# Performance work log

Measured on AMD Instinct MI355X. Metric: run time of the kernel, lower is better.

Reference implementation:

```python
import jax, jax.numpy as jnp
import numpy as np

T, LDIMS, HID, HID2 = 768, 256, 512, 512


def setup_inputs() -> dict:
    key = jax.random.key(0)
    ks = jax.random.split(key, 8)
    s = 0.05  # small init scale keeps tanh out of saturation
    return {
        "x": jax.random.normal(ks[0], (T, 2, LDIMS), dtype=jnp.float32),
        "hidLayerFOH": jax.random.normal(ks[1], (2 * LDIMS, HID), dtype=jnp.float32) * s,
        "hidLayerFOM": jax.random.normal(ks[2], (2 * LDIMS, HID), dtype=jnp.float32) * s,
        "catBias": jax.random.normal(ks[3], (2 * HID,), dtype=jnp.float32) * s,
        "hid2Layer": jax.random.normal(ks[4], (2 * HID, HID2), dtype=jnp.float32) * s,
        "hid2Bias": jax.random.normal(ks[5], (HID2,), dtype=jnp.float32) * s,
        "outLayer": jax.random.normal(ks[6], (HID2, 1), dtype=jnp.float32) * s,
        "outBias": jax.random.normal(ks[7], (1,), dtype=jnp.float32) * s,
    }


def reference(x, hidLayerFOH, hidLayerFOM, catBias, hid2Layer, hid2Bias, outLayer, outBias):
    # x: [T, 2, ldims] -> concat forward/backward LSTM states -> [T, 2*ldims]
    xc = x.reshape(x.shape[0], -1)
    Hf = xc @ hidLayerFOH  # [T, HID] headfov per token
    Mf = xc @ hidLayerFOM  # [T, HID] modfov per token
    # Original: tanh(concat([headfov_i, modfov_j]) + catBias) @ hid2Layer.
    # tanh is elementwise, so split the concat: act halves separately, then
    # split hid2Layer into top/bottom blocks — same math, no [T,T,2H] tensor.
    actH = jnp.tanh(Hf + catBias[:HID])   # [T, HID]
    actM = jnp.tanh(Mf + catBias[HID:])   # [T, HID]
    AH = actH @ hid2Layer[:HID]           # [T, HID2]
    AM = actM @ hid2Layer[HID:]           # [T, HID2]
    # Pairwise second layer: Z[i,j] = tanh(AH[i] + AM[j] + hid2Bias)
    Z = jnp.tanh(AH[:, None, :] + AM[None, :, :] + hid2Bias)  # [T, T, HID2]
    scores = jnp.einsum("ijh,h->ij", Z, outLayer[:, 0]) + outBias[0]  # [T, T]
    return scores
```

## Files before the change

kernel.cpp:

```cpp
#include <hip/hip_runtime.h>

#define TT 768
#define KD 512
#define NC 1024
#define RLN2_2 2.8853900817779268f

typedef short short8 __attribute__((ext_vector_type(8)));
typedef float f32x4  __attribute__((ext_vector_type(4)));
typedef float f32x2  __attribute__((ext_vector_type(2)));

__device__ __forceinline__ float fast_exp2(float x) {
#if __has_builtin(__builtin_amdgcn_exp2f)
    return __builtin_amdgcn_exp2f(x);
#else
    return exp2f(x);
#endif
}
__device__ __forceinline__ float fast_rcp(float x) {
#if __has_builtin(__builtin_amdgcn_rcpf)
    return __builtin_amdgcn_rcpf(x);
#else
    return 1.0f / x;
#endif
}
__device__ __forceinline__ float fast_tanh(float x) {
    float e = fast_exp2(x * RLN2_2);
    return fmaf(-2.0f, fast_rcp(e + 1.0f), 1.0f);
}
__device__ __forceinline__ ushort f2bf(float f) {
    uint u = __float_as_uint(f);
    u += 0x7fff + ((u >> 16) & 1);
    return (ushort)(u >> 16);
}

__global__ __launch_bounds__(128) void k_gemm1(
    const float* __restrict__ x, const float* __restrict__ foh,
    const float* __restrict__ fom, const float* __restrict__ catBias,
    ushort* __restrict__ act)
{
    __shared__ float ps[64][20];
    __shared__ float bt[2][32][33];

    const int t = threadIdx.x;
    const int kv = t >> 6, lane = t & 63;
    const int n0 = blockIdx.x * 32;
    const int m0 = blockIdx.y * 32;
    const float* B = (n0 < 512) ? foh : fom;
    const int nc0  = (n0 < 512) ? n0 : n0 - 512;
    const int lrow = lane & 15, lk = (lane >> 4) * 8;
    const int kbase = kv * 256;

    const int skr = lane >> 1;
    const int snc = (lane & 1) * 16;

    const float* px0 = &x[(m0 + lrow) * KD + kbase + lk];
    const float* px1 = px0 + 16 * KD;

    f32x4 acc[2][2] = {};
    #pragma unroll 1
    for (int c = 0; c < 8; ++c) {
        const int k0 = kbase + c * 32;
        const float* bsrc = &B[(k0 + skr) * 512 + nc0 + snc];
        float4 s0 = *(const float4*)(bsrc);
        float4 s1 = *(const float4*)(bsrc + 4);
        float4 s2 = *(const float4*)(bsrc + 8);
        float4 s3 = *(const float4*)(bsrc + 12);
        *(float4*)&bt[kv][skr][snc]      = s0;
        *(float4*)&bt[kv][skr][snc + 4]  = s1;
        *(float4*)&bt[kv][skr][snc + 8]  = s2;
        *(float4*)&bt[kv][skr][snc + 12] = s3;
        float4 a00 = *(const float4*)(px0 + c * 32);
        float4 a01 = *(const float4*)(px0 + c * 32 + 4);
        float4 a10 = *(const float4*)(px1 + c * 32);
        float4 a11 = *(const float4*)(px1 + c * 32 + 4);
        short8 af0, af1;
        af0[0] = (short)f2bf(a00.x); af0[1] = (short)f2bf(a00.y);
        af0[2] = (short)f2bf(a00.z); af0[3] = (short)f2bf(a00.w);
        af0[4] = (short)f2bf(a01.x); af0[5] = (short)f2bf(a01.y);
        af0[6] = (short)f2bf(a01.z); af0[7] = (short)f2bf(a01.w);
        af1[0] = (short)f2bf(a10.x); af1[1] = (short)f2bf(a10.y);
        af1[2] = (short)f2bf(a10.z); af1[3] = (short)f2bf(a10.w);
        af1[4] = (short)f2bf(a11.x); af1[5] = (short)f2bf(a11.y);
        af1[6] = (short)f2bf(a11.z); af1[7] = (short)f2bf(a11.w);
        short8 bf0, bf1;
        #pragma unroll
        for (int q = 0; q < 8; ++q) {
            bf0[q] = (short)f2bf(bt[kv][lk + q][lrow]);
            bf1[q] = (short)f2bf(bt[kv][lk + q][lrow + 16]);
        }
        acc[0][0] = __builtin_amdgcn_mfma_f32_16x16x32_bf16(af0, bf0, acc[0][0], 0, 0, 0);
        acc[0][1] = __builtin_amdgcn_mfma_f32_16x16x32_bf16(af0, bf1, acc[0][1], 0, 0, 0);
        acc[1][0] = __builtin_amdgcn_mfma_f32_16x16x32_bf16(af1, bf0, acc[1][0], 0, 0, 0);
        acc[1][1] = __builtin_amdgcn_mfma_f32_16x16x32_bf16(af1, bf1, acc[1][1], 0, 0, 0);
    }
    if (kv == 1) {
        *(f32x4*)&ps[lane][0]  = acc[0][0];
        *(f32x4*)&ps[lane][4]  = acc[0][1];
        *(f32x4*)&ps[lane][8]  = acc[1][0];
        *(f32x4*)&ps[lane][12] = acc[1][1];
    }
    __syncthreads();
    if (kv == 0) {
        acc[0][0] += *(const f32x4*)&ps[lane][0];
        acc[0][1] += *(const f32x4*)&ps[lane][4];
        acc[1][0] += *(const f32x4*)&ps[lane][8];
        acc[1][1] += *(const f32x4*)&ps[lane][12];
        const int crow = (lane >> 4) * 4, ccol = lane & 15;
        #pragma unroll
        for (int nf = 0; nf < 2; ++nf) {
            int col = n0 + nf * 16 + ccol;
            float cb = catBias[col];
            #pragma unroll
            for (int mf = 0; mf < 2; ++mf) {
                #pragma unroll
                for (int r = 0; r < 4; ++r) {
                    int row = m0 + mf * 16 + crow + r;
                    act[row * NC + col] = f2bf(fast_tanh(acc[mf][nf][r] + cb));
                }
            }
        }
    }
}

__global__ __launch_bounds__(128) void k_gemm2(
    const ushort* __restrict__ act, const float* __restrict__ hid2,
    const float* __restrict__ hid2Bias, float* __restrict__ pw)
{
    __shared__ float ps[64][20];
    __shared__ float bt[2][32][33];

    const int t = threadIdx.x;
    const int kv = t >> 6, lane = t & 63;
    const int n0 = blockIdx.x * 32;
    const int m0 = blockIdx.y * 32;
    const bool top = (blockIdx.x < 16);
    const int koff = top ? 0 : 512;
    const int nc0  = top ? n0 : n0 - 512;
    const int lrow = lane & 15, lk = (lane >> 4) * 8;
    const int kbase = kv * 256;

    const int skr = lane >> 1;
    const int snc = (lane & 1) * 16;

    const ushort* pa0 = &act[(m0 + lrow) * NC + koff + kbase + lk];
    const ushort* pa1 = pa0 + 16 * NC;

    f32x4 acc[2][2] = {};
    #pragma unroll 1
    for (int c = 0; c < 8; ++c) {
        const int k0 = kbase + c * 32;
        const float* bsrc = &hid2[(koff + k0 + skr) * 512 + nc0 + snc];
        float4 s0 = *(const float4*)(bsrc);
        float4 s1 = *(const float4*)(bsrc + 4);
        float4 s2 = *(const float4*)(bsrc + 8);
        float4 s3 = *(const float4*)(bsrc + 12);
        *(float4*)&bt[kv][skr][snc]      = s0;
        *(float4*)&bt[kv][skr][snc + 4]  = s1;
        *(float4*)&bt[kv][skr][snc + 8]  = s2;
        *(float4*)&bt[kv][skr][snc + 12] = s3;
        short8 af0 = *(const short8*)(pa0 + c * 32);
        short8 af1 = *(const short8*)(pa1 + c * 32);
        short8 bf0, bf1;
        #pragma unroll
        for (int q = 0; q < 8; ++q) {
            bf0[q] = (short)f2bf(bt[kv][lk + q][lrow]);
            bf1[q] = (short)f2bf(bt[kv][lk + q][lrow + 16]);
        }
        acc[0][0] = __builtin_amdgcn_mfma_f32_16x16x32_bf16(af0, bf0, acc[0][0], 0, 0, 0);
        acc[0][1] = __builtin_amdgcn_mfma_f32_16x16x32_bf16(af0, bf1, acc[0][1], 0, 0, 0);
        acc[1][0] = __builtin_amdgcn_mfma_f32_16x16x32_bf16(af1, bf0, acc[1][0], 0, 0, 0);
        acc[1][1] = __builtin_amdgcn_mfma_f32_16x16x32_bf16(af1, bf1, acc[1][1], 0, 0, 0);
    }
    if (kv == 1) {
        *(f32x4*)&ps[lane][0]  = acc[0][0];
        *(f32x4*)&ps[lane][4]  = acc[0][1];
        *(f32x4*)&ps[lane][8]  = acc[1][0];
        *(f32x4*)&ps[lane][12] = acc[1][1];
    }
    __syncthreads();
    if (kv == 0) {
        acc[0][0] += *(const f32x4*)&ps[lane][0];
        acc[0][1] += *(const f32x4*)&ps[lane][4];
        acc[1][0] += *(const f32x4*)&ps[lane][8];
        acc[1][1] += *(const f32x4*)&ps[lane][12];
        const int crow = (lane >> 4) * 4, ccol = lane & 15;
        #pragma unroll
        for (int nf = 0; nf < 2; ++nf) {
            int col = n0 + nf * 16 + ccol;
            float hb = top ? hid2Bias[col] : 0.0f;
            #pragma unroll
            for (int mf = 0; mf < 2; ++mf) {
                #pragma unroll
                for (int r = 0; r < 4; ++r) {
                    int row = m0 + mf * 16 + crow + r;
                    pw[row * NC + col] = fast_exp2(RLN2_2 * (acc[mf][nf][r] + hb));
                }
            }
        }
    }
}

__global__ __launch_bounds__(256) void k_pair(
    const float* __restrict__ pw, const float* __restrict__ w,
    const float* __restrict__ outBias, float* __restrict__ out)
{
    __shared__ float Ea[4][16][18];
    __shared__ float Em[4][16][18];
    __shared__ float wl[512];

    const int t    = threadIdx.x;
    const int wv   = t >> 6, lane = t & 63;
    const int bid  = blockIdx.x;
    const int sw   = (bid & 7) * 288 + (bid >> 3);
    const int it = sw / 48, jt = sw % 48;
    const int i0 = it * 16, j0 = jt * 16;
    const int hb0 = wv * 128;

    *(float2*)&wl[hb0 + lane * 2] = *(const float2*)&w[hb0 + lane * 2];
    float4 wa = *(const float4*)&w[lane * 8];
    float4 wb = *(const float4*)&w[lane * 8 + 4];
    float lsum = (wa.x + wa.y) + (wa.z + wa.w) + (wb.x + wb.y) + (wb.z + wb.w);
    #pragma unroll
    for (int d = 1; d < 64; d <<= 1) lsum += __shfl_xor(lsum, d, 64);

    const int sr = lane >> 2;
    const int sc = (lane & 3) * 4;
    const float* srcA = &pw[(i0 + sr) * NC + hb0 + sc];
    const float* srcM = &pw[(j0 + sr) * NC + 512 + hb0 + sc];

    const int li = lane >> 3, lj = lane & 7;

    float4 fa = *(const float4*)(srcA);
    float4 fm = *(const float4*)(srcM);

    const f32x2 one2 = {1.0f, 1.0f};
    f32x2 accA[2] = {}, accB[2] = {};

    #pragma unroll 1
    for (int c = 0; c < 8; ++c) {
        const int hh = c * 16;
        *(float4*)&Ea[wv][sr][sc] = fa;
        *(float4*)&Em[wv][sr][sc] = fm;
        if (c < 7) {
            fa = *(const float4*)(srcA + hh + 16);
            fm = *(const float4*)(srcM + hh + 16);
        }
        #pragma unroll
        for (int hq = 0; hq < 4; ++hq) {
            float4 e0 = *(const float4*)&Ea[wv][2 * li    ][hq * 4];
            float4 e1 = *(const float4*)&Ea[wv][2 * li + 1][hq * 4];
            float4 f0 = *(const float4*)&Em[wv][2 * lj    ][hq * 4];
            float4 f1 = *(const float4*)&Em[wv][2 * lj + 1][hq * 4];
            float4 w4 = *(const float4*)&wl[hb0 + hh + hq * 4];
            #define PKQUAD(DA, DB, WH, ACCA, ACCB)                   \
            {                                                        \
                f32x2 Q  = DA * DB;                                  \
                float pr = Q.x * Q.y;                                \
                float R  = fast_rcp(pr);                             \
                float RW = R * (WH);                                 \
                f32x2 T  = (f32x2){Q.y, Q.x} * RW;                   \
                ACCA = __builtin_elementwise_fma(T, DB, ACCA);       \
                ACCB = __builtin_elementwise_fma(T, DA, ACCB);       \
            }
            #define HSTEP(H, S)                                                     \
            {                                                                       \
                f32x2 F  = {f0.H, f1.H};                                            \
                f32x2 D0 = __builtin_elementwise_fma((f32x2){e0.H, e0.H}, F, one2); \
                f32x2 D1 = __builtin_elementwise_fma((f32x2){e1.H, e1.H}, F, one2); \
                PKQUAD(D0, D1, w4.H, accA[S], accB[S])                              \
            }
            HSTEP(x, 0) HSTEP(y, 1) HSTEP(z, 0) HSTEP(w, 1)
            #undef HSTEP
            #undef PKQUAD
        }
    }

    f32x2 s0 = accA[0] + accA[1];
    f32x2 s1 = accB[0] + accB[1];

    float* partial = (float*)Ea;
    __syncthreads();
    if (wv >= 1) {
        float* p = partial + (wv - 1) * 256 + lane * 4;
        p[0] = s0.x; p[1] = s0.y; p[2] = s1.x; p[3] = s1.y;
    }
    __syncthreads();
    if (wv == 0) {
        const float base = lsum + outBias[0];
        float t00 = s0.x, t01 = s0.y, t10 = s1.x, t11 = s1.y;
        #pragma unroll
        for (int q = 0; q < 3; ++q) {
            const float* p = partial + q * 256 + lane * 4;
            t00 += p[0]; t01 += p[1]; t10 += p[2]; t11 += p[3];
        }
        const int gi = i0 + 2 * li, gj = j0 + 2 * lj;
        float2 o0, o1;
        o0.x = fmaf(-2.f, t00, base);
        o0.y = fmaf(-2.f, t01, base);
        o1.x = fmaf(-2.f, t10, base);
        o1.y = fmaf(-2.f, t11, base);
        *(float2*)&out[gi * TT + gj]       = o0;
        *(float2*)&out[(gi + 1) * TT + gj] = o1;
    }
}

extern "C" void kernel_launch(void* const* d_in, const int* in_sizes, int n_in,
                              void* d_out, int out_size, void* d_ws, size_t ws_size,
                              hipStream_t stream) {
    const float* x        = (const float*)d_in[0];
    const float* foh      = (const float*)d_in[1];
    const float* fom      = (const float*)d_in[2];
    const float* catBias  = (const float*)d_in[3];
    const float* hid2     = (const float*)d_in[4];
    const float* hid2Bias = (const float*)d_in[5];
    const float* outLayer = (const float*)d_in[6];
    const float* outBias  = (const float*)d_in[7];
    float* out = (float*)d_out;

    char* wsb = (char*)d_ws;
    float*  pw  = (float*)(wsb);
    ushort* act = (ushort*)(wsb + 3145728);

    k_gemm1<<<dim3(32, 24), 128, 0, stream>>>(x, foh, fom, catBias, act);
    k_gemm2<<<dim3(32, 24), 128, 0, stream>>>(act, hid2, hid2Bias, pw);
    k_pair <<<dim3(2304),   256, 0, stream>>>(pw, outLayer, outBias, out);
}
```

Measured before the change: 55.37 us.

## Enlarge pair tile to 16x32 so each thread computes 2x4 outputs

The pairwise kernel now tiles 16 i-rows by 32 j-columns per block, with each lane computing a 2x4 output patch instead of 2x2, and launches half as many blocks. Each lane reuses the loaded e values across four f values, which cuts shared-memory reads per output and amortizes the weight load and the cross-wave reduction. The rcp-pairing trick now groups the two j-pairs for the same i. The costs are more registers, fewer blocks, and a larger LDS footprint for the Em buffer.

```diff
diff --git a/kernel.cpp b/kernel.cpp
--- a/kernel.cpp
+++ b/kernel.cpp
@@ -205,15 +205,15 @@
     const float* __restrict__ outBias, float* __restrict__ out)
 {
     __shared__ float Ea[4][16][18];
-    __shared__ float Em[4][16][18];
+    __shared__ float Em[4][32][18];
     __shared__ float wl[512];
 
     const int t    = threadIdx.x;
     const int wv   = t >> 6, lane = t & 63;
     const int bid  = blockIdx.x;
-    const int sw   = (bid & 7) * 288 + (bid >> 3);
-    const int it = sw / 48, jt = sw % 48;
-    const int i0 = it * 16, j0 = jt * 16;
+    const int sw   = (bid & 7) * 144 + (bid >> 3);
+    const int it = sw / 24, jt = sw % 24;
+    const int i0 = it * 16, j0 = jt * 32;
     const int hb0 = wv * 128;
 
     *(float2*)&wl[hb0 + lane * 2] = *(const float2*)&w[hb0 + lane * 2];
@@ -223,84 +223,101 @@
     #pragma unroll
     for (int d = 1; d < 64; d <<= 1) lsum += __shfl_xor(lsum, d, 64);
 
-    const int sr = lane >> 2;
-    const int sc = (lane & 3) * 4;
-    const float* srcA = &pw[(i0 + sr) * NC + hb0 + sc];
-    const float* srcM = &pw[(j0 + sr) * NC + 512 + hb0 + sc];
+    const int sr  = lane >> 2, sc  = (lane & 3) * 4;
+    const int smr = lane >> 1, smc = (lane & 1) * 8;
+    const float* srcA = &pw[(i0 + sr)  * NC + hb0 + sc];
+    const float* srcM = &pw[(j0 + smr) * NC + 512 + hb0 + smc];
 
     const int li = lane >> 3, lj = lane & 7;
 
-    float4 fa = *(const float4*)(srcA);
-    float4 fm = *(const float4*)(srcM);
+    float4 fa  = *(const float4*)(srcA);
+    float4 fm0 = *(const float4*)(srcM);
+    float4 fm1 = *(const float4*)(srcM + 4);
 
     const f32x2 one2 = {1.0f, 1.0f};
-    f32x2 accA[2] = {}, accB[2] = {};
+    f32x2 aA01[2] = {}, aA23[2] = {};
+    f32x2 aB01[2] = {}, aB23[2] = {};
 
     #pragma unroll 1
     for (int c = 0; c < 8; ++c) {
         const int hh = c * 16;
-        *(float4*)&Ea[wv][sr][sc] = fa;
-        *(float4*)&Em[wv][sr][sc] = fm;
+        *(float4*)&Ea[wv][sr][sc]        = fa;
+        *(float4*)&Em[wv][smr][smc]      = fm0;
+        *(float4*)&Em[wv][smr][smc + 4]  = fm1;
         if (c < 7) {
-            fa = *(const float4*)(srcA + hh + 16);
-            fm = *(const float4*)(srcM + hh + 16);
+            fa  = *(const float4*)(srcA + hh + 16);
+            fm0 = *(const float4*)(srcM + hh + 16);
+            fm1 = *(const float4*)(srcM + hh + 20);
         }
         #pragma unroll
         for (int hq = 0; hq < 4; ++hq) {
             float4 e0 = *(const float4*)&Ea[wv][2 * li    ][hq * 4];
             float4 e1 = *(const float4*)&Ea[wv][2 * li + 1][hq * 4];
-            float4 f0 = *(const float4*)&Em[wv][2 * lj    ][hq * 4];
-            float4 f1 = *(const float4*)&Em[wv][2 * lj + 1][hq * 4];
+            float4 f0 = *(const float4*)&Em[wv][4 * lj    ][hq * 4];
+            float4 f1 = *(const float4*)&Em[wv][4 * lj + 1][hq * 4];
+            float4 f2 = *(const float4*)&Em[wv][4 * lj + 2][hq * 4];
+            float4 f3 = *(const float4*)&Em[wv][4 * lj + 3][hq * 4];
             float4 w4 = *(const float4*)&wl[hb0 + hh + hq * 4];
-            #define PKQUAD(DA, DB, WH, ACCA, ACCB)                   \
-            {                                                        \
-                f32x2 Q  = DA * DB;                                  \
-                float pr = Q.x * Q.y;                                \
-                float R  = fast_rcp(pr);                             \
-                float RW = R * (WH);                                 \
-                f32x2 T  = (f32x2){Q.y, Q.x} * RW;                   \
-                ACCA = __builtin_elementwise_fma(T, DB, ACCA);       \
-                ACCB = __builtin_elementwise_fma(T, DA, ACCB);       \
+            #define ROWQ(EH, WH, A01, A23)                                   \
+            {                                                                \
+                f32x2 E  = {EH, EH};                                         \
+                f32x2 DA = __builtin_elementwise_fma(E, F01, one2);          \
+                f32x2 DB = __builtin_elementwise_fma(E, F23, one2);          \
+                f32x2 Q  = DA * DB;                                          \
+                float R  = fast_rcp(Q.x * Q.y);                              \
+                float RW = R * (WH);                                         \
+                f32x2 T2 = (f32x2){Q.y, Q.x} * RW;                           \
+                A01 = __builtin_elementwise_fma(T2, DB, A01);                \
+                A23 = __builtin_elementwise_fma(T2, DA, A23);                \
             }
-            #define HSTEP(H, S)                                                     \
-            {                                                                       \
-                f32x2 F  = {f0.H, f1.H};                                            \
-                f32x2 D0 = __builtin_elementwise_fma((f32x2){e0.H, e0.H}, F, one2); \
-                f32x2 D1 = __builtin_elementwise_fma((f32x2){e1.H, e1.H}, F, one2); \
-                PKQUAD(D0, D1, w4.H, accA[S], accB[S])                              \
+            #define HSTEP(H, S)                                              \
+            {                                                                \
+                f32x2 F01 = {f0.H, f1.H};                                    \
+                f32x2 F23 = {f2.H, f3.H};                                    \
+                ROWQ(e0.H, w4.H, aA01[S], aA23[S])                           \
+                ROWQ(e1.H, w4.H, aB01[S], aB23[S])                           \
             }
             HSTEP(x, 0) HSTEP(y, 1) HSTEP(z, 0) HSTEP(w, 1)
             #undef HSTEP
-            #undef PKQUAD
-        }
-    }
-
-    f32x2 s0 = accA[0] + accA[1];
-    f32x2 s1 = accB[0] + accB[1];
-
-    float* partial = (float*)Ea;
+            #undef ROWQ
+        }
+    }
+
+    f32x2 sA01 = aA01[0] + aA01[1];
+    f32x2 sA23 = aA23[0] + aA23[1];
+    f32x2 sB01 = aB01[0] + aB01[1];
+    f32x2 sB23 = aB23[0] + aB23[1];
+
+    float* partial = (float*)Em;
     __syncthreads();
     if (wv >= 1) {
-        float* p = partial + (wv - 1) * 256 + lane * 4;
-        p[0] = s0.x; p[1] = s0.y; p[2] = s1.x; p[3] = s1.y;
+        float* p = partial + (wv - 1) * 512 + lane * 8;
+        p[0] = sA01.x; p[1] = sA01.y; p[2] = sA23.x; p[3] = sA23.y;
+        p[4] = sB01.x; p[5] = sB01.y; p[6] = sB23.x; p[7] = sB23.y;
     }
     __syncthreads();
     if (wv == 0) {
         const float base = lsum + outBias[0];
-        float t00 = s0.x, t01 = s0.y, t10 = s1.x, t11 = s1.y;
+        float tt[8] = {sA01.x, sA01.y, sA23.x, sA23.y,
+                       sB01.x, sB01.y, sB23.x, sB23.y};
         #pragma unroll
         for (int q = 0; q < 3; ++q) {
-            const float* p = partial + q * 256 + lane * 4;
-            t00 += p[0]; t01 += p[1]; t10 += p[2]; t11 += p[3];
-        }
-        const int gi = i0 + 2 * li, gj = j0 + 2 * lj;
-        float2 o0, o1;
-        o0.x = fmaf(-2.f, t00, base);
-        o0.y = fmaf(-2.f, t01, base);
-        o1.x = fmaf(-2.f, t10, base);
-        o1.y = fmaf(-2.f, t11, base);
-        *(float2*)&out[gi * TT + gj]       = o0;
-        *(float2*)&out[(gi + 1) * TT + gj] = o1;
+            const float* p = partial + q * 512 + lane * 8;
+            #pragma unroll
+            for (int k = 0; k < 8; ++k) tt[k] += p[k];
+        }
+        const int gi = i0 + 2 * li, gj = j0 + 4 * lj;
+        float4 o0, o1;
+        o0.x = fmaf(-2.f, tt[0], base);
+        o0.y = fmaf(-2.f, tt[1], base);
+        o0.z = fmaf(-2.f, tt[2], base);
+        o0.w = fmaf(-2.f, tt[3], base);
+        o1.x = fmaf(-2.f, tt[4], base);
+        o1.y = fmaf(-2.f, tt[5], base);
+        o1.z = fmaf(-2.f, tt[6], base);
+        o1.w = fmaf(-2.f, tt[7], base);
+        *(float4*)&out[gi * TT + gj]       = o0;
+        *(float4*)&out[(gi + 1) * TT + gj] = o1;
     }
 }
 
@@ -323,5 +340,5 @@
 
     k_gemm1<<<dim3(32, 24), 128, 0, stream>>>(x, foh, fom, catBias, act);
     k_gemm2<<<dim3(32, 24), 128, 0, stream>>>(act, hid2, hid2Bias, pw);
-    k_pair <<<dim3(2304),   256, 0, stream>>>(pw, outLayer, outBias, out);
-}
+    k_pair <<<dim3(1152),   256, 0, stream>>>(pw, outLayer, outBias, out);
+}
```

New measurement: 56.95 us. 1.03x slower.
